# Performance work log

Hardware: AMD Instinct MI355X
Metric: run time of the kernel (lower is better)

Reference implementation:

```python
import jax, jax.numpy as jnp
import numpy as np

L, B, D = 2048, 8, 1024


def setup_inputs() -> dict:
    key = jax.random.key(0)
    ks = jax.random.split(key, 10)
    s = 0.02  # Linear weight scale to keep exp(k) in a sane range
    return {
        "x": jax.random.normal(ks[0], (L, B, D), jnp.float32),
        "mu_k": jax.random.uniform(ks[1], (D,), jnp.float32),
        "mu_v": jax.random.uniform(ks[2], (D,), jnp.float32),
        "mu_r": jax.random.uniform(ks[3], (D,), jnp.float32),
        "Wk": jax.random.normal(ks[4], (D, D), jnp.float32) * s,
        "Wv": jax.random.normal(ks[5], (D, D), jnp.float32) * s,
        "Wr": jax.random.normal(ks[6], (D, D), jnp.float32) * s,
        "W_out": jax.random.normal(ks[7], (D, D), jnp.float32) * s,
        "w": jax.random.uniform(ks[8], (D,), jnp.float32),
        "u": jax.random.uniform(ks[9], (D,), jnp.float32),
    }


def reference(x, mu_k, mu_v, mu_r, Wk, Wv, Wr, W_out, w, u):
    # x: [L, B, D] (time-first). Fresh hidden state => numerator/denominator_last = 0.
    Lx = x.shape[0]
    # PreviousMixing (RWKV token shift): mu*x_t + (1-mu)*x_{t-1}, zero initial prev.
    x_prev = jnp.concatenate([jnp.zeros_like(x[:1]), x[:-1]], axis=0)
    k = (mu_k * x + (1.0 - mu_k) * x_prev) @ Wk.T
    v = (mu_v * x + (1.0 - mu_v) * x_prev) @ Wv.T
    r = (mu_r * x + (1.0 - mu_r) * x_prev) @ Wr.T

    w_neg = -jnp.exp(w)                      # [D], negative decay
    exp_w = jnp.exp(w_neg)                   # [D]
    t = jnp.arange(Lx, dtype=x.dtype)
    ewp = jnp.exp(w_neg[None, :] * t[:, None])  # [L, D] decay progression

    exp_k = jnp.exp(k)                       # [L, B, D]
    exp_k_v = exp_k * v

    n = 2 * Lx  # zero-padded FFT length for linear convolution
    f_ewp = jnp.fft.rfft(ewp, n=n, axis=0)[:, None, :]        # [n/2+1, 1, D]
    f_ek = jnp.fft.rfft(exp_k, n=n, axis=0)                   # [n/2+1, B, D]
    f_ekv = jnp.fft.rfft(exp_k_v, n=n, axis=0)
    conv_ek = jnp.fft.irfft(f_ewp * f_ek, axis=0)[:Lx]         # [L, B, D]
    conv_ekv = jnp.fft.irfft(f_ewp * f_ekv, axis=0)[:Lx]

    # Initial numerator_last/denominator_last are zeros, so their terms vanish.
    denominator = conv_ek
    numerator = conv_ekv

    exp_u = jnp.exp(u)
    denominator_out = (denominator - exp_k) / exp_w + exp_k * exp_u
    numerator_out = (numerator - exp_k_v) / exp_w + exp_k_v * exp_u
    return (jax.nn.sigmoid(r) * numerator_out / denominator_out) @ W_out.T
```

## Files before the change

kernel.cpp:

```cpp
#include <hip/hip_runtime.h>
#include <cstddef>
#include <cstdint>

#define Lq 2048
#define Bq 8
#define Dq 1024
#define Mq (Lq*Bq)

typedef _Float16 f16;
typedef _Float16 f16x2 __attribute__((ext_vector_type(2)));
typedef _Float16 f16x8 __attribute__((ext_vector_type(8)));
typedef float f32x4 __attribute__((ext_vector_type(4)));

typedef const __attribute__((address_space(1))) uint32_t GU32;
typedef __attribute__((address_space(3))) uint32_t LU32;

#define BAR()    asm volatile("s_barrier" ::: "memory")
#define WAITV4() asm volatile("s_waitcnt vmcnt(4)" ::: "memory")

__global__ __launch_bounds__(256) void cvt3_k(const float* __restrict__ a,
                                              const float* __restrict__ b,
                                              const float* __restrict__ c,
                                              f16* __restrict__ dst) {
  int i = (blockIdx.x * 256 + threadIdx.x) * 8;
  const float* s = (blockIdx.y == 0) ? a : (blockIdx.y == 1) ? b : c;
  f16* d = dst + (size_t)blockIdx.y * ((size_t)Dq * Dq) + i;
  float4 v0 = *(const float4*)(s + i);
  float4 v1 = *(const float4*)(s + i + 4);
  f16x8 o;
  o[0] = (f16)v0.x; o[1] = (f16)v0.y; o[2] = (f16)v0.z; o[3] = (f16)v0.w;
  o[4] = (f16)v1.x; o[5] = (f16)v1.y; o[6] = (f16)v1.z; o[7] = (f16)v1.w;
  *(f16x8*)d = o;
}

__global__ __launch_bounds__(256) void cvt1_k(const float* __restrict__ s,
                                              f16* __restrict__ d) {
  int i = (blockIdx.x * 256 + threadIdx.x) * 8;
  float4 v0 = *(const float4*)(s + i);
  float4 v1 = *(const float4*)(s + i + 4);
  f16x8 o;
  o[0] = (f16)v0.x; o[1] = (f16)v0.y; o[2] = (f16)v0.z; o[3] = (f16)v0.w;
  o[4] = (f16)v1.x; o[5] = (f16)v1.y; o[6] = (f16)v1.z; o[7] = (f16)v1.w;
  *(f16x8*)(d + i) = o;
}

__global__ __launch_bounds__(256) void prep_k(const float* __restrict__ x,
                                              const float* __restrict__ muk,
                                              const float* __restrict__ muv,
                                              const float* __restrict__ mur,
                                              f16* __restrict__ xk,
                                              f16* __restrict__ xv,
                                              f16* __restrict__ xr) {
  const size_t base0 = ((size_t)blockIdx.x * 256 + threadIdx.x) * 8;
  const int col = (int)(base0 & (Dq - 1));

  float mk[8], mv[8], mr[8];
#define LD8(MU, DST)                                                           \
  { float4 m0 = *(const float4*)((MU) + col);                                  \
    float4 m1 = *(const float4*)((MU) + col + 4);                              \
    DST[0]=m0.x; DST[1]=m0.y; DST[2]=m0.z; DST[3]=m0.w;                        \
    DST[4]=m1.x; DST[5]=m1.y; DST[6]=m1.z; DST[7]=m1.w; }
  LD8(muk, mk) LD8(muv, mv) LD8(mur, mr)
#undef LD8

#pragma unroll
  for (int it = 0; it < 4; ++it) {
    size_t i = base0 + (size_t)it * (8u * 524288u);
    float4 a0 = *(const float4*)(x + i);
    float4 a1 = *(const float4*)(x + i + 4);
    float4 p0 = make_float4(0.f, 0.f, 0.f, 0.f), p1 = p0;
    if (i >= (size_t)(Bq * Dq)) {
      p0 = *(const float4*)(x + i - Bq * Dq);
      p1 = *(const float4*)(x + i - Bq * Dq + 4);
    }
    float av[8] = {a0.x, a0.y, a0.z, a0.w, a1.x, a1.y, a1.z, a1.w};
    float pv[8] = {p0.x, p0.y, p0.z, p0.w, p1.x, p1.y, p1.z, p1.w};
#define MIX8(MV, DST)                                                          \
    { f16x8 o;                                                                 \
      _Pragma("unroll")                                                        \
      for (int j = 0; j < 8; ++j) o[j] = (f16)(pv[j] + MV[j] * (av[j] - pv[j]));\
      *(f16x8*)((DST) + i) = o; }
    MIX8(mk, xk)
    MIX8(mv, xv)
    MIX8(mr, xr)
#undef MIX8
  }
}

template<int OUTF32>
__device__ __forceinline__ void gemm_core(const f16* __restrict__ A,
                                          const f16* __restrict__ W,
                                          void* __restrict__ Cv,
                                          int bx, int by) {
  __shared__ f16 lds[2][2][256][64];
  const int tid  = threadIdx.x;
  const int lane = tid & 63;
  const int wid  = tid >> 6;
  const int wr   = wid >> 2;
  const int wc   = wid & 3;

  const int fr = lane & 15;
  const int fg = lane >> 4;
  const int c0 = ((fg    ) ^ (fr & 7)) * 8;
  const int c1 = ((fg ^ 4) ^ (fr & 7)) * 8;

  const int rowoff = wid * 8 + (lane >> 3);
  const int scol   = ((lane & 7) ^ (lane >> 3)) * 8;
  const f16* Ab = A + (size_t)(by * 256) * Dq;
  const f16* Wb = W + (size_t)(bx * 256) * Dq;

#define STAGE(bufi, op, h, base, kt) do {                                      \
    const f16* _g = (base) + (size_t)((h) * 128 + rowoff) * Dq + (kt) * 64 + scol; \
    __builtin_amdgcn_global_load_lds((GU32*)_g,                                \
        (LU32*)&lds[bufi][op][(h) * 128 + wid * 8][0], 16, 0, 0);              \
    __builtin_amdgcn_global_load_lds((GU32*)(_g + (size_t)64 * Dq),            \
        (LU32*)&lds[bufi][op][(h) * 128 + 64 + wid * 8][0], 16, 0, 0);         \
  } while (0)

  f16x8 af[4][2], bf0[2][2], bf1[2][2];
  f32x4 acc[8][4] = {};

#define LOAD_A(bufi, mh)                                                       \
  _Pragma("unroll")                                                            \
  for (int mi2 = 0; mi2 < 4; ++mi2) {                                          \
    af[mi2][0] = *(const f16x8*)&lds[bufi][0][wr * 128 + (mh) * 64 + mi2 * 16 + fr][c0]; \
    af[mi2][1] = *(const f16x8*)&lds[bufi][0][wr * 128 + (mh) * 64 + mi2 * 16 + fr][c1]; \
  }
#define LOAD_B(bufi, nh, bf)                                                   \
  _Pragma("unroll")                                                            \
  for (int ni2 = 0; ni2 < 2; ++ni2) {                                          \
    bf[ni2][0] = *(const f16x8*)&lds[bufi][1][wc * 64 + (nh) * 32 + ni2 * 16 + fr][c0]; \
    bf[ni2][1] = *(const f16x8*)&lds[bufi][1][wc * 64 + (nh) * 32 + ni2 * 16 + fr][c1]; \
  }
#define MFMA_Q(mh, nh, bf)                                                     \
  __builtin_amdgcn_s_setprio(1);                                               \
  _Pragma("unroll")                                                            \
  for (int ks = 0; ks < 2; ++ks)                                               \
    _Pragma("unroll")                                                          \
    for (int mi2 = 0; mi2 < 4; ++mi2)                                          \
      _Pragma("unroll")                                                        \
      for (int ni2 = 0; ni2 < 2; ++ni2)                                        \
        acc[(mh) * 4 + mi2][(nh) * 2 + ni2] =                                  \
            __builtin_amdgcn_mfma_f32_16x16x32_f16(af[mi2][ks], bf[ni2][ks],   \
                acc[(mh) * 4 + mi2][(nh) * 2 + ni2], 0, 0, 0);                 \
  __builtin_amdgcn_s_setprio(0);

  STAGE(0, 0, 0, Ab, 0); STAGE(0, 0, 1, Ab, 0);
  STAGE(0, 1, 0, Wb, 0); STAGE(0, 1, 1, Wb, 0);
  STAGE(1, 1, 0, Wb, 1); STAGE(1, 1, 1, Wb, 1);
  WAITV4();
  BAR();

  for (int i = 0; i < 8; ++i) {
    const int t1 = 2 * i + 1;
    int t2 = 2 * i + 2; if (t2 > 15) t2 = 15;
    int t3 = 2 * i + 3; if (t3 > 15) t3 = 15;
    LOAD_A(0, 0); LOAD_B(0, 0, bf0);
    STAGE(1, 0, 0, Ab, t1);
    BAR(); MFMA_Q(0, 0, bf0); BAR();
    LOAD_B(0, 1, bf1);
    STAGE(1, 0, 1, Ab, t1);
    BAR(); MFMA_Q(0, 1, bf1); BAR();
    LOAD_A(0, 1);
    STAGE(0, 1, 0, Wb, t2);
    BAR(); MFMA_Q(1, 1, bf1); BAR();
    STAGE(0, 1, 1, Wb, t2);
    BAR(); MFMA_Q(1, 0, bf0); WAITV4(); BAR();
    LOAD_A(1, 0); LOAD_B(1, 0, bf0);
    STAGE(0, 0, 0, Ab, t2);
    BAR(); MFMA_Q(0, 0, bf0); BAR();
    LOAD_B(1, 1, bf1);
    STAGE(0, 0, 1, Ab, t2);
    BAR(); MFMA_Q(0, 1, bf1); BAR();
    LOAD_A(1, 1);
    STAGE(1, 1, 0, Wb, t3);
    BAR(); MFMA_Q(1, 1, bf1); BAR();
    STAGE(1, 1, 1, Wb, t3);
    BAR(); MFMA_Q(1, 0, bf0); WAITV4(); BAR();
  }

#pragma unroll
  for (int mi = 0; mi < 8; ++mi) {
    const int row0 = by * 256 + wr * 128 + mi * 16 + fg * 4;
#pragma unroll
    for (int ni = 0; ni < 4; ++ni) {
      const int col = bx * 256 + wc * 64 + ni * 16 + fr;
      if (OUTF32) {
        float* C = (float*)Cv;
#pragma unroll
        for (int j = 0; j < 4; ++j)
          C[(size_t)(row0 + j) * Dq + col] = acc[mi][ni][j];
      } else {
        f16* C = (f16*)Cv;
#pragma unroll
        for (int j = 0; j < 4; ++j)
          C[(size_t)(row0 + j) * Dq + col] = (f16)acc[mi][ni][j];
      }
    }
  }
#undef STAGE
#undef LOAD_A
#undef LOAD_B
#undef MFMA_Q
}

__global__ __launch_bounds__(512, 2) void gemm3_k(const f16* __restrict__ xr,
                                                  const f16* __restrict__ xv,
                                                  const f16* __restrict__ xk,
                                                  const f16* __restrict__ w16,
                                                  f16* __restrict__ rb,
                                                  f16* __restrict__ vb,
                                                  f16* __restrict__ kb) {
  const int s = blockIdx.x >> 8;
  const int inner = blockIdx.x & 255;
  const int wg = (inner & 7) * 32 + (inner >> 3);
  const f16* A = (s == 0) ? xr : (s == 1) ? xv : xk;
  const f16* W = w16 + (size_t)s * Dq * Dq;
  f16* C = (s == 0) ? rb : (s == 1) ? vb : kb;
  gemm_core<0>(A, W, C, wg & 3, wg >> 2);
}

__global__ __launch_bounds__(512, 2) void gemmO_k(const f16* __restrict__ A,
                                                  const f16* __restrict__ W,
                                                  float* __restrict__ C) {
  const int wg = (blockIdx.x & 7) * 32 + (blockIdx.x >> 3);
  gemm_core<1>(A, W, C, wg & 3, wg >> 2);
}

constexpr int CHUNK = 32, LOOKBACK = 16;

__global__ __launch_bounds__(256) void scan_k(const f16* __restrict__ kk,
                                              const f16* __restrict__ vv,
                                              const f16* rr,
                                              const float* __restrict__ w,
                                              const float* __restrict__ u,
                                              f16* y) {
  const int unit = blockIdx.y * 256 + threadIdx.x;
  const int d = (unit & 511) * 2;
  const int b = unit >> 9;
  const int t0 = blockIdx.x * CHUNK;

  const float dec0 = __expf(-__expf(w[d]));
  const float dec1 = __expf(-__expf(w[d + 1]));
  const float eu0  = __expf(u[d]);
  const float eu1  = __expf(u[d + 1]);

  float A0 = 0.f, A1 = 0.f, Av0 = 0.f, Av1 = 0.f;
  const size_t base = (size_t)b * Dq + d;

  if (t0 > 0) {
#pragma unroll
    for (int t = t0 - LOOKBACK; t < t0; ++t) {
      size_t idx = (size_t)t * (Bq * Dq) + base;
      f16x2 k2 = *(const f16x2*)(kk + idx);
      f16x2 v2 = *(const f16x2*)(vv + idx);
      float ek0 = __expf((float)k2[0]), ek1 = __expf((float)k2[1]);
      A0  = fmaf(dec0, A0,  ek0);
      A1  = fmaf(dec1, A1,  ek1);
      Av0 = fmaf(dec0, Av0, ek0 * (float)v2[0]);
      Av1 = fmaf(dec1, Av1, ek1 * (float)v2[1]);
    }
  }
#pragma unroll
  for (int t = t0; t < t0 + CHUNK; ++t) {
    size_t idx = (size_t)t * (Bq * Dq) + base;
    f16x2 k2 = *(const f16x2*)(kk + idx);
    f16x2 v2 = *(const f16x2*)(vv + idx);
    f16x2 r2 = *(const f16x2*)(rr + idx);
    float ek0 = __expf((float)k2[0]), ek1 = __expf((float)k2[1]);
    float ekv0 = ek0 * (float)v2[0], ekv1 = ek1 * (float)v2[1];
    float den0 = fmaf(ek0,  eu0, A0),  den1 = fmaf(ek1,  eu1, A1);
    float num0 = fmaf(ekv0, eu0, Av0), num1 = fmaf(ekv1, eu1, Av1);
    float s0 = __builtin_amdgcn_rcpf(1.f + __expf(-(float)r2[0]));
    float s1 = __builtin_amdgcn_rcpf(1.f + __expf(-(float)r2[1]));
    f16x2 o;
    o[0] = (f16)(s0 * num0 * __builtin_amdgcn_rcpf(den0));
    o[1] = (f16)(s1 * num1 * __builtin_amdgcn_rcpf(den1));
    *(f16x2*)(y + idx) = o;
    A0  = fmaf(dec0, A0,  ek0);
    A1  = fmaf(dec1, A1,  ek1);
    Av0 = fmaf(dec0, Av0, ekv0);
    Av1 = fmaf(dec1, Av1, ekv1);
  }
}

extern "C" void kernel_launch(void* const* d_in, const int* in_sizes, int n_in,
                              void* d_out, int out_size, void* d_ws, size_t ws_size,
                              hipStream_t stream) {
  const float* x    = (const float*)d_in[0];
  const float* mu_k = (const float*)d_in[1];
  const float* mu_v = (const float*)d_in[2];
  const float* mu_r = (const float*)d_in[3];
  const float* Wk   = (const float*)d_in[4];
  const float* Wv   = (const float*)d_in[5];
  const float* Wr   = (const float*)d_in[6];
  const float* Wo   = (const float*)d_in[7];
  const float* w    = (const float*)d_in[8];
  const float* u    = (const float*)d_in[9];

  f16* xk = (f16*)d_ws;
  f16* xv = xk + (size_t)Mq * Dq;
  f16* xr = xv + (size_t)Mq * Dq;
  f16* kb = xr + (size_t)Mq * Dq;
  f16* vb = kb + (size_t)Mq * Dq;
  f16* rb = vb + (size_t)Mq * Dq;
  f16* w16  = (f16*)d_out;
  f16* wo16 = xk;

  cvt3_k<<<dim3(512, 3), 256, 0, stream>>>(Wr, Wv, Wk, w16);
  prep_k<<<2048, 256, 0, stream>>>(x, mu_k, mu_v, mu_r, xk, xv, xr);
  gemm3_k<<<768, 512, 0, stream>>>(xr, xv, xk, w16, rb, vb, kb);
  cvt1_k<<<512, 256, 0, stream>>>(Wo, wo16);
  scan_k<<<dim3(Lq / CHUNK, 16), 256, 0, stream>>>(kb, vb, rb, w, u, rb);
  gemmO_k<<<256, 512, 0, stream>>>(rb, wo16, (float*)d_out);
}
```

Before: 218.2 us.

## Interleave r/v/k inputs and weights so one block computes all three projections

The three mixed activations and the three projection weights are now stored interleaved along a 3072-wide row, and the first GEMM launches 256 blocks instead of 768. Each block loops over the three projections, streams K-tiles continuously across projection boundaries and writes each output before resetting its accumulators. This cuts block launch and prologue overhead and keeps the pipeline running through the transitions. In exchange it gives a third as many blocks, one wave at 256 workgroups, so there is less parallel slack and the tail or load balance could get worse.

```diff
diff --git a/kernel.cpp b/kernel.cpp
--- a/kernel.cpp
+++ b/kernel.cpp
@@ -6,6 +6,7 @@
 #define Bq 8
 #define Dq 1024
 #define Mq (Lq*Bq)
+#define K3 3072
 
 typedef _Float16 f16;
 typedef _Float16 f16x2 __attribute__((ext_vector_type(2)));
@@ -21,10 +22,11 @@
 __global__ __launch_bounds__(256) void cvt3_k(const float* __restrict__ a,
                                               const float* __restrict__ b,
                                               const float* __restrict__ c,
-                                              f16* __restrict__ dst) {
+                                              f16* __restrict__ w3) {
   int i = (blockIdx.x * 256 + threadIdx.x) * 8;
   const float* s = (blockIdx.y == 0) ? a : (blockIdx.y == 1) ? b : c;
-  f16* d = dst + (size_t)blockIdx.y * ((size_t)Dq * Dq) + i;
+  int n = i >> 10, col = i & (Dq - 1);
+  f16* d = w3 + (size_t)n * K3 + blockIdx.y * Dq + col;
   float4 v0 = *(const float4*)(s + i);
   float4 v1 = *(const float4*)(s + i + 4);
   f16x8 o;
@@ -48,9 +50,7 @@
                                               const float* __restrict__ muk,
                                               const float* __restrict__ muv,
                                               const float* __restrict__ mur,
-                                              f16* __restrict__ xk,
-                                              f16* __restrict__ xv,
-                                              f16* __restrict__ xr) {
+                                              f16* __restrict__ x3) {
   const size_t base0 = ((size_t)blockIdx.x * 256 + threadIdx.x) * 8;
   const int col = (int)(base0 & (Dq - 1));
 
@@ -65,7 +65,9 @@
 
 #pragma unroll
   for (int it = 0; it < 4; ++it) {
-    size_t i = base0 + (size_t)it * (8u * 524288u);
+    size_t i = base0 + (size_t)it * 4194304u;
+    size_t m = i >> 10;
+    f16* dst = x3 + m * K3 + col;
     float4 a0 = *(const float4*)(x + i);
     float4 a1 = *(const float4*)(x + i + 4);
     float4 p0 = make_float4(0.f, 0.f, 0.f, 0.f), p1 = p0;
@@ -75,22 +77,22 @@
     }
     float av[8] = {a0.x, a0.y, a0.z, a0.w, a1.x, a1.y, a1.z, a1.w};
     float pv[8] = {p0.x, p0.y, p0.z, p0.w, p1.x, p1.y, p1.z, p1.w};
-#define MIX8(MV, DST)                                                          \
+#define MIX8(MV, OFF)                                                          \
     { f16x8 o;                                                                 \
       _Pragma("unroll")                                                        \
       for (int j = 0; j < 8; ++j) o[j] = (f16)(pv[j] + MV[j] * (av[j] - pv[j]));\
-      *(f16x8*)((DST) + i) = o; }
-    MIX8(mk, xk)
-    MIX8(mv, xv)
-    MIX8(mr, xr)
+      *(f16x8*)(dst + (OFF)) = o; }
+    MIX8(mr, 0)
+    MIX8(mv, Dq)
+    MIX8(mk, 2 * Dq)
 #undef MIX8
   }
 }
 
-template<int OUTF32>
+template<int OUTF32, int NEP, int AST>
 __device__ __forceinline__ void gemm_core(const f16* __restrict__ A,
                                           const f16* __restrict__ W,
-                                          void* __restrict__ Cv,
+                                          void* c0v, void* c1v, void* c2v,
                                           int bx, int by) {
   __shared__ f16 lds[2][2][256][64];
   const int tid  = threadIdx.x;
@@ -106,14 +108,15 @@
 
   const int rowoff = wid * 8 + (lane >> 3);
   const int scol   = ((lane & 7) ^ (lane >> 3)) * 8;
-  const f16* Ab = A + (size_t)(by * 256) * Dq;
-  const f16* Wb = W + (size_t)(bx * 256) * Dq;
+  const f16* Ab = A + (size_t)(by * 256) * AST;
+  const f16* Wb = W + (size_t)(bx * 256) * AST;
+  const int NT = NEP * 16;
 
 #define STAGE(bufi, op, h, base, kt) do {                                      \
-    const f16* _g = (base) + (size_t)((h) * 128 + rowoff) * Dq + (kt) * 64 + scol; \
+    const f16* _g = (base) + (size_t)((h) * 128 + rowoff) * AST + (kt) * 64 + scol; \
     __builtin_amdgcn_global_load_lds((GU32*)_g,                                \
         (LU32*)&lds[bufi][op][(h) * 128 + wid * 8][0], 16, 0, 0);              \
-    __builtin_amdgcn_global_load_lds((GU32*)(_g + (size_t)64 * Dq),            \
+    __builtin_amdgcn_global_load_lds((GU32*)(_g + (size_t)64 * AST),           \
         (LU32*)&lds[bufi][op][(h) * 128 + 64 + wid * 8][0], 16, 0, 0);         \
   } while (0)
 
@@ -151,50 +154,54 @@
   WAITV4();
   BAR();
 
-  for (int i = 0; i < 8; ++i) {
-    const int t1 = 2 * i + 1;
-    int t2 = 2 * i + 2; if (t2 > 15) t2 = 15;
-    int t3 = 2 * i + 3; if (t3 > 15) t3 = 15;
-    LOAD_A(0, 0); LOAD_B(0, 0, bf0);
-    STAGE(1, 0, 0, Ab, t1);
-    BAR(); MFMA_Q(0, 0, bf0); BAR();
-    LOAD_B(0, 1, bf1);
-    STAGE(1, 0, 1, Ab, t1);
-    BAR(); MFMA_Q(0, 1, bf1); BAR();
-    LOAD_A(0, 1);
-    STAGE(0, 1, 0, Wb, t2);
-    BAR(); MFMA_Q(1, 1, bf1); BAR();
-    STAGE(0, 1, 1, Wb, t2);
-    BAR(); MFMA_Q(1, 0, bf0); WAITV4(); BAR();
-    LOAD_A(1, 0); LOAD_B(1, 0, bf0);
-    STAGE(0, 0, 0, Ab, t2);
-    BAR(); MFMA_Q(0, 0, bf0); BAR();
-    LOAD_B(1, 1, bf1);
-    STAGE(0, 0, 1, Ab, t2);
-    BAR(); MFMA_Q(0, 1, bf1); BAR();
-    LOAD_A(1, 1);
-    STAGE(1, 1, 0, Wb, t3);
-    BAR(); MFMA_Q(1, 1, bf1); BAR();
-    STAGE(1, 1, 1, Wb, t3);
-    BAR(); MFMA_Q(1, 0, bf0); WAITV4(); BAR();
-  }
-
-#pragma unroll
-  for (int mi = 0; mi < 8; ++mi) {
-    const int row0 = by * 256 + wr * 128 + mi * 16 + fg * 4;
-#pragma unroll
-    for (int ni = 0; ni < 4; ++ni) {
-      const int col = bx * 256 + wc * 64 + ni * 16 + fr;
-      if (OUTF32) {
-        float* C = (float*)Cv;
-#pragma unroll
-        for (int j = 0; j < 4; ++j)
-          C[(size_t)(row0 + j) * Dq + col] = acc[mi][ni][j];
-      } else {
-        f16* C = (f16*)Cv;
-#pragma unroll
-        for (int j = 0; j < 4; ++j)
-          C[(size_t)(row0 + j) * Dq + col] = (f16)acc[mi][ni][j];
+  for (int e = 0; e < NEP; ++e) {
+    for (int i = 0; i < 8; ++i) {
+      const int g = e * 8 + i;
+      const int t1 = 2 * g + 1;
+      int t2 = 2 * g + 2; if (t2 > NT - 1) t2 = NT - 1;
+      int t3 = 2 * g + 3; if (t3 > NT - 1) t3 = NT - 1;
+      LOAD_A(0, 0); LOAD_B(0, 0, bf0);
+      STAGE(1, 0, 0, Ab, t1);
+      BAR(); MFMA_Q(0, 0, bf0); BAR();
+      LOAD_B(0, 1, bf1);
+      STAGE(1, 0, 1, Ab, t1);
+      BAR(); MFMA_Q(0, 1, bf1); BAR();
+      LOAD_A(0, 1);
+      STAGE(0, 1, 0, Wb, t2);
+      BAR(); MFMA_Q(1, 1, bf1); BAR();
+      STAGE(0, 1, 1, Wb, t2);
+      BAR(); MFMA_Q(1, 0, bf0); WAITV4(); BAR();
+      LOAD_A(1, 0); LOAD_B(1, 0, bf0);
+      STAGE(0, 0, 0, Ab, t2);
+      BAR(); MFMA_Q(0, 0, bf0); BAR();
+      LOAD_B(1, 1, bf1);
+      STAGE(0, 0, 1, Ab, t2);
+      BAR(); MFMA_Q(0, 1, bf1); BAR();
+      LOAD_A(1, 1);
+      STAGE(1, 1, 0, Wb, t3);
+      BAR(); MFMA_Q(1, 1, bf1); BAR();
+      STAGE(1, 1, 1, Wb, t3);
+      BAR(); MFMA_Q(1, 0, bf0); WAITV4(); BAR();
+    }
+    void* Cv = (e == 0) ? c0v : (e == 1) ? c1v : c2v;
+#pragma unroll
+    for (int mi = 0; mi < 8; ++mi) {
+      const int row0 = by * 256 + wr * 128 + mi * 16 + fg * 4;
+#pragma unroll
+      for (int ni = 0; ni < 4; ++ni) {
+        const int col = bx * 256 + wc * 64 + ni * 16 + fr;
+        if (OUTF32) {
+          float* C = (float*)Cv;
+#pragma unroll
+          for (int j = 0; j < 4; ++j)
+            C[(size_t)(row0 + j) * Dq + col] = acc[mi][ni][j];
+        } else {
+          f16* C = (f16*)Cv;
+#pragma unroll
+          for (int j = 0; j < 4; ++j)
+            C[(size_t)(row0 + j) * Dq + col] = (f16)acc[mi][ni][j];
+        }
+        acc[mi][ni] = (f32x4){0.f, 0.f, 0.f, 0.f};
       }
     }
   }
@@ -204,27 +211,20 @@
 #undef MFMA_Q
 }
 
-__global__ __launch_bounds__(512, 2) void gemm3_k(const f16* __restrict__ xr,
-                                                  const f16* __restrict__ xv,
-                                                  const f16* __restrict__ xk,
-                                                  const f16* __restrict__ w16,
+__global__ __launch_bounds__(512, 2) void gemm3_k(const f16* __restrict__ x3,
+                                                  const f16* __restrict__ w3,
                                                   f16* __restrict__ rb,
                                                   f16* __restrict__ vb,
                                                   f16* __restrict__ kb) {
-  const int s = blockIdx.x >> 8;
-  const int inner = blockIdx.x & 255;
-  const int wg = (inner & 7) * 32 + (inner >> 3);
-  const f16* A = (s == 0) ? xr : (s == 1) ? xv : xk;
-  const f16* W = w16 + (size_t)s * Dq * Dq;
-  f16* C = (s == 0) ? rb : (s == 1) ? vb : kb;
-  gemm_core<0>(A, W, C, wg & 3, wg >> 2);
+  const int wg = (blockIdx.x & 7) * 32 + (blockIdx.x >> 3);
+  gemm_core<0, 3, K3>(x3, w3, rb, vb, kb, wg & 3, wg >> 2);
 }
 
 __global__ __launch_bounds__(512, 2) void gemmO_k(const f16* __restrict__ A,
                                                   const f16* __restrict__ W,
                                                   float* __restrict__ C) {
   const int wg = (blockIdx.x & 7) * 32 + (blockIdx.x >> 3);
-  gemm_core<1>(A, W, C, wg & 3, wg >> 2);
+  gemm_core<1, 1, Dq>(A, W, C, nullptr, nullptr, wg & 3, wg >> 2);
 }
 
 constexpr int CHUNK = 32, LOOKBACK = 16;
@@ -298,18 +298,16 @@
   const float* w    = (const float*)d_in[8];
   const float* u    = (const float*)d_in[9];
 
-  f16* xk = (f16*)d_ws;
-  f16* xv = xk + (size_t)Mq * Dq;
-  f16* xr = xv + (size_t)Mq * Dq;
-  f16* kb = xr + (size_t)Mq * Dq;
+  f16* x3 = (f16*)d_ws;
+  f16* kb = x3 + (size_t)Mq * K3;
   f16* vb = kb + (size_t)Mq * Dq;
   f16* rb = vb + (size_t)Mq * Dq;
-  f16* w16  = (f16*)d_out;
-  f16* wo16 = xk;
-
-  cvt3_k<<<dim3(512, 3), 256, 0, stream>>>(Wr, Wv, Wk, w16);
-  prep_k<<<2048, 256, 0, stream>>>(x, mu_k, mu_v, mu_r, xk, xv, xr);
-  gemm3_k<<<768, 512, 0, stream>>>(xr, xv, xk, w16, rb, vb, kb);
+  f16* w3   = (f16*)d_out;
+  f16* wo16 = x3;
+
+  cvt3_k<<<dim3(512, 3), 256, 0, stream>>>(Wr, Wv, Wk, w3);
+  prep_k<<<2048, 256, 0, stream>>>(x, mu_k, mu_v, mu_r, x3);
+  gemm3_k<<<256, 512, 0, stream>>>(x3, w3, rb, vb, kb);
   cvt1_k<<<512, 256, 0, stream>>>(Wo, wo16);
   scan_k<<<dim3(Lq / CHUNK, 16), 256, 0, stream>>>(kb, vb, rb, w, u, rb);
   gemmO_k<<<256, 512, 0, stream>>>(rb, wo16, (float*)d_out);
```

Result: slower. 234.3 us (+7.4%).

## Restructure GEMM mainloop to 4-slot K=32 LDS pipeline with prefetch depth three

Applied to the files above, without the earlier changes.

The f16 GEMM core now uses four LDS ring slots of 256x32 tiles for A and B instead of two 256x64 buffers. Loads run three K-steps ahead and the wait count is raised to vmcnt(8). Fragment loads and MFMA phases are reorganised to one k-slice per phase with a new XOR swizzle. The aim is to hide global-load latency better with deeper prefetch, at the cost of more barriers per unit of K work and smaller MFMA bursts between syncs.

```diff
diff --git a/kernel.cpp b/kernel.cpp
--- a/kernel.cpp
+++ b/kernel.cpp
@@ -16,7 +16,7 @@
 typedef __attribute__((address_space(3))) uint32_t LU32;
 
 #define BAR()    asm volatile("s_barrier" ::: "memory")
-#define WAITV4() asm volatile("s_waitcnt vmcnt(4)" ::: "memory")
+#define WAITV8() asm volatile("s_waitcnt vmcnt(8)" ::: "memory")
 
 __global__ __launch_bounds__(256) void cvt3_k(const float* __restrict__ a,
                                               const float* __restrict__ b,
@@ -65,7 +65,7 @@
 
 #pragma unroll
   for (int it = 0; it < 4; ++it) {
-    size_t i = base0 + (size_t)it * (8u * 524288u);
+    size_t i = base0 + (size_t)it * 4194304u;
     float4 a0 = *(const float4*)(x + i);
     float4 a1 = *(const float4*)(x + i + 4);
     float4 p0 = make_float4(0.f, 0.f, 0.f, 0.f), p1 = p0;
@@ -92,7 +92,8 @@
                                           const f16* __restrict__ W,
                                           void* __restrict__ Cv,
                                           int bx, int by) {
-  __shared__ f16 lds[2][2][256][64];
+  __shared__ f16 As[4][256][32];
+  __shared__ f16 Bs[4][256][32];
   const int tid  = threadIdx.x;
   const int lane = tid & 63;
   const int wid  = tid >> 6;
@@ -101,82 +102,67 @@
 
   const int fr = lane & 15;
   const int fg = lane >> 4;
-  const int c0 = ((fg    ) ^ (fr & 7)) * 8;
-  const int c1 = ((fg ^ 4) ^ (fr & 7)) * 8;
-
-  const int rowoff = wid * 8 + (lane >> 3);
-  const int scol   = ((lane & 7) ^ (lane >> 3)) * 8;
-  const f16* Ab = A + (size_t)(by * 256) * Dq;
-  const f16* Wb = W + (size_t)(bx * 256) * Dq;
-
-#define STAGE(bufi, op, h, base, kt) do {                                      \
-    const f16* _g = (base) + (size_t)((h) * 128 + rowoff) * Dq + (kt) * 64 + scol; \
-    __builtin_amdgcn_global_load_lds((GU32*)_g,                                \
-        (LU32*)&lds[bufi][op][(h) * 128 + wid * 8][0], 16, 0, 0);              \
-    __builtin_amdgcn_global_load_lds((GU32*)(_g + (size_t)64 * Dq),            \
-        (LU32*)&lds[bufi][op][(h) * 128 + 64 + wid * 8][0], 16, 0, 0);         \
+  const int cA = (fg ^ ((fr >> 1) & 3)) * 8;
+
+  const int s_r = wid * 16 + (lane >> 2);
+  const int s_c = ((lane & 3) ^ ((lane >> 3) & 3)) * 8;
+  const f16* Ag = A + ((size_t)(by * 256 + s_r)) * Dq + s_c;
+  const f16* Wg = W + ((size_t)(bx * 256 + s_r)) * Dq + s_c;
+
+#define STAGE_A(slot, kt) do {                                                 \
+    __builtin_amdgcn_global_load_lds((GU32*)(Ag + (kt) * 32),                  \
+        (LU32*)&As[slot][wid * 16][0], 16, 0, 0);                              \
+    __builtin_amdgcn_global_load_lds((GU32*)(Ag + (size_t)128 * Dq + (kt) * 32),\
+        (LU32*)&As[slot][128 + wid * 16][0], 16, 0, 0);                        \
   } while (0)
-
-  f16x8 af[4][2], bf0[2][2], bf1[2][2];
+#define STAGE_B(slot, kt) do {                                                 \
+    __builtin_amdgcn_global_load_lds((GU32*)(Wg + (kt) * 32),                  \
+        (LU32*)&Bs[slot][wid * 16][0], 16, 0, 0);                              \
+    __builtin_amdgcn_global_load_lds((GU32*)(Wg + (size_t)128 * Dq + (kt) * 32),\
+        (LU32*)&Bs[slot][128 + wid * 16][0], 16, 0, 0);                        \
+  } while (0)
+
+  f16x8 af[4], bf[4];
   f32x4 acc[8][4] = {};
 
-#define LOAD_A(bufi, mh)                                                       \
+#define LOAD_A4(slot, mh)                                                      \
   _Pragma("unroll")                                                            \
-  for (int mi2 = 0; mi2 < 4; ++mi2) {                                          \
-    af[mi2][0] = *(const f16x8*)&lds[bufi][0][wr * 128 + (mh) * 64 + mi2 * 16 + fr][c0]; \
-    af[mi2][1] = *(const f16x8*)&lds[bufi][0][wr * 128 + (mh) * 64 + mi2 * 16 + fr][c1]; \
-  }
-#define LOAD_B(bufi, nh, bf)                                                   \
+  for (int mi2 = 0; mi2 < 4; ++mi2)                                            \
+    af[mi2] = *(const f16x8*)&As[slot][wr * 128 + (mh) * 64 + mi2 * 16 + fr][cA];
+#define LOAD_B4(slot)                                                          \
   _Pragma("unroll")                                                            \
-  for (int ni2 = 0; ni2 < 2; ++ni2) {                                          \
-    bf[ni2][0] = *(const f16x8*)&lds[bufi][1][wc * 64 + (nh) * 32 + ni2 * 16 + fr][c0]; \
-    bf[ni2][1] = *(const f16x8*)&lds[bufi][1][wc * 64 + (nh) * 32 + ni2 * 16 + fr][c1]; \
-  }
-#define MFMA_Q(mh, nh, bf)                                                     \
+  for (int ni2 = 0; ni2 < 4; ++ni2)                                            \
+    bf[ni2] = *(const f16x8*)&Bs[slot][wc * 64 + ni2 * 16 + fr][cA];
+#define MFMA_PH(mh)                                                            \
   __builtin_amdgcn_s_setprio(1);                                               \
   _Pragma("unroll")                                                            \
-  for (int ks = 0; ks < 2; ++ks)                                               \
+  for (int mi2 = 0; mi2 < 4; ++mi2)                                            \
     _Pragma("unroll")                                                          \
-    for (int mi2 = 0; mi2 < 4; ++mi2)                                          \
-      _Pragma("unroll")                                                        \
-      for (int ni2 = 0; ni2 < 2; ++ni2)                                        \
-        acc[(mh) * 4 + mi2][(nh) * 2 + ni2] =                                  \
-            __builtin_amdgcn_mfma_f32_16x16x32_f16(af[mi2][ks], bf[ni2][ks],   \
-                acc[(mh) * 4 + mi2][(nh) * 2 + ni2], 0, 0, 0);                 \
+    for (int ni2 = 0; ni2 < 4; ++ni2)                                          \
+      acc[(mh) * 4 + mi2][ni2] =                                               \
+          __builtin_amdgcn_mfma_f32_16x16x32_f16(af[mi2], bf[ni2],             \
+              acc[(mh) * 4 + mi2][ni2], 0, 0, 0);                              \
   __builtin_amdgcn_s_setprio(0);
 
-  STAGE(0, 0, 0, Ab, 0); STAGE(0, 0, 1, Ab, 0);
-  STAGE(0, 1, 0, Wb, 0); STAGE(0, 1, 1, Wb, 0);
-  STAGE(1, 1, 0, Wb, 1); STAGE(1, 1, 1, Wb, 1);
-  WAITV4();
+  STAGE_A(0, 0); STAGE_B(0, 0);
+  STAGE_A(1, 1); STAGE_B(1, 1);
+  STAGE_A(2, 2); STAGE_B(2, 2);
+  WAITV8();
   BAR();
 
-  for (int i = 0; i < 8; ++i) {
-    const int t1 = 2 * i + 1;
-    int t2 = 2 * i + 2; if (t2 > 15) t2 = 15;
-    int t3 = 2 * i + 3; if (t3 > 15) t3 = 15;
-    LOAD_A(0, 0); LOAD_B(0, 0, bf0);
-    STAGE(1, 0, 0, Ab, t1);
-    BAR(); MFMA_Q(0, 0, bf0); BAR();
-    LOAD_B(0, 1, bf1);
-    STAGE(1, 0, 1, Ab, t1);
-    BAR(); MFMA_Q(0, 1, bf1); BAR();
-    LOAD_A(0, 1);
-    STAGE(0, 1, 0, Wb, t2);
-    BAR(); MFMA_Q(1, 1, bf1); BAR();
-    STAGE(0, 1, 1, Wb, t2);
-    BAR(); MFMA_Q(1, 0, bf0); WAITV4(); BAR();
-    LOAD_A(1, 0); LOAD_B(1, 0, bf0);
-    STAGE(0, 0, 0, Ab, t2);
-    BAR(); MFMA_Q(0, 0, bf0); BAR();
-    LOAD_B(1, 1, bf1);
-    STAGE(0, 0, 1, Ab, t2);
-    BAR(); MFMA_Q(0, 1, bf1); BAR();
-    LOAD_A(1, 1);
-    STAGE(1, 1, 0, Wb, t3);
-    BAR(); MFMA_Q(1, 1, bf1); BAR();
-    STAGE(1, 1, 1, Wb, t3);
-    BAR(); MFMA_Q(1, 0, bf0); WAITV4(); BAR();
+  for (int tt = 0; tt < 8; ++tt) {
+#pragma unroll
+    for (int q = 0; q < 4; ++q) {
+      const int t = tt * 4 + q;
+      int st = t + 3; if (st > 31) st = 31;
+      const int ss = (q + 3) & 3;
+      LOAD_A4(q, 0); LOAD_B4(q);
+      STAGE_A(ss, st);
+      BAR(); MFMA_PH(0); BAR();
+      LOAD_A4(q, 1);
+      STAGE_B(ss, st);
+      BAR(); MFMA_PH(1); WAITV8(); BAR();
+    }
   }
 
 #pragma unroll
@@ -198,10 +184,11 @@
       }
     }
   }
-#undef STAGE
-#undef LOAD_A
-#undef LOAD_B
-#undef MFMA_Q
+#undef STAGE_A
+#undef STAGE_B
+#undef LOAD_A4
+#undef LOAD_B4
+#undef MFMA_PH
 }
 
 __global__ __launch_bounds__(512, 2) void gemm3_k(const f16* __restrict__ xr,
```

Result: slower. 228.2 us (+4.6%).

## Fold weight conversion into prep kernel and retile output GEMM to 128x256

Applied to the files above, without the earlier changes.

The separate fp32-to-fp16 conversion of Wr/Wv/Wk is merged into the token-shift prep kernel as extra blocks, removing one launch. The output projection GEMM gets its own kernel with 128x256 tiles, K-step 32, double-buffered global-to-LDS loads and a smaller LDS footprint. It launches 512 workgroups instead of 256, which is meant to fill the CUs better. Smaller tiles give less data reuse per workgroup in exchange.

```diff
diff --git a/kernel.cpp b/kernel.cpp
--- a/kernel.cpp
+++ b/kernel.cpp
@@ -17,41 +17,34 @@
 
 #define BAR()    asm volatile("s_barrier" ::: "memory")
 #define WAITV4() asm volatile("s_waitcnt vmcnt(4)" ::: "memory")
-
-__global__ __launch_bounds__(256) void cvt3_k(const float* __restrict__ a,
-                                              const float* __restrict__ b,
-                                              const float* __restrict__ c,
-                                              f16* __restrict__ dst) {
-  int i = (blockIdx.x * 256 + threadIdx.x) * 8;
-  const float* s = (blockIdx.y == 0) ? a : (blockIdx.y == 1) ? b : c;
-  f16* d = dst + (size_t)blockIdx.y * ((size_t)Dq * Dq) + i;
-  float4 v0 = *(const float4*)(s + i);
-  float4 v1 = *(const float4*)(s + i + 4);
-  f16x8 o;
-  o[0] = (f16)v0.x; o[1] = (f16)v0.y; o[2] = (f16)v0.z; o[3] = (f16)v0.w;
-  o[4] = (f16)v1.x; o[5] = (f16)v1.y; o[6] = (f16)v1.z; o[7] = (f16)v1.w;
-  *(f16x8*)d = o;
-}
-
-__global__ __launch_bounds__(256) void cvt1_k(const float* __restrict__ s,
-                                              f16* __restrict__ d) {
-  int i = (blockIdx.x * 256 + threadIdx.x) * 8;
-  float4 v0 = *(const float4*)(s + i);
-  float4 v1 = *(const float4*)(s + i + 4);
-  f16x8 o;
-  o[0] = (f16)v0.x; o[1] = (f16)v0.y; o[2] = (f16)v0.z; o[3] = (f16)v0.w;
-  o[4] = (f16)v1.x; o[5] = (f16)v1.y; o[6] = (f16)v1.z; o[7] = (f16)v1.w;
-  *(f16x8*)(d + i) = o;
-}
+#define WAITV3() asm volatile("s_waitcnt vmcnt(3)" ::: "memory")
 
 __global__ __launch_bounds__(256) void prep_k(const float* __restrict__ x,
                                               const float* __restrict__ muk,
                                               const float* __restrict__ muv,
                                               const float* __restrict__ mur,
+                                              const float* __restrict__ Wr,
+                                              const float* __restrict__ Wv,
+                                              const float* __restrict__ Wk,
                                               f16* __restrict__ xk,
                                               f16* __restrict__ xv,
-                                              f16* __restrict__ xr) {
-  const size_t base0 = ((size_t)blockIdx.x * 256 + threadIdx.x) * 8;
+                                              f16* __restrict__ xr,
+                                              f16* __restrict__ w16) {
+  const int bid = blockIdx.x;
+  if (bid < 1536) {
+    int y = bid >> 9;
+    int i = ((bid & 511) * 256 + threadIdx.x) * 8;
+    const float* s = (y == 0) ? Wr : (y == 1) ? Wv : Wk;
+    f16* d = w16 + (size_t)y * ((size_t)Dq * Dq) + i;
+    float4 v0 = *(const float4*)(s + i);
+    float4 v1 = *(const float4*)(s + i + 4);
+    f16x8 o;
+    o[0] = (f16)v0.x; o[1] = (f16)v0.y; o[2] = (f16)v0.z; o[3] = (f16)v0.w;
+    o[4] = (f16)v1.x; o[5] = (f16)v1.y; o[6] = (f16)v1.z; o[7] = (f16)v1.w;
+    *(f16x8*)d = o;
+    return;
+  }
+  const size_t base0 = ((size_t)(bid - 1536) * 256 + threadIdx.x) * 8;
   const int col = (int)(base0 & (Dq - 1));
 
   float mk[8], mv[8], mr[8];
@@ -65,7 +58,7 @@
 
 #pragma unroll
   for (int it = 0; it < 4; ++it) {
-    size_t i = base0 + (size_t)it * (8u * 524288u);
+    size_t i = base0 + (size_t)it * 4194304u;
     float4 a0 = *(const float4*)(x + i);
     float4 a1 = *(const float4*)(x + i + 4);
     float4 p0 = make_float4(0.f, 0.f, 0.f, 0.f), p1 = p0;
@@ -87,11 +80,21 @@
   }
 }
 
-template<int OUTF32>
-__device__ __forceinline__ void gemm_core(const f16* __restrict__ A,
-                                          const f16* __restrict__ W,
-                                          void* __restrict__ Cv,
-                                          int bx, int by) {
+__global__ __launch_bounds__(256) void cvt1_k(const float* __restrict__ s,
+                                              f16* __restrict__ d) {
+  int i = (blockIdx.x * 256 + threadIdx.x) * 8;
+  float4 v0 = *(const float4*)(s + i);
+  float4 v1 = *(const float4*)(s + i + 4);
+  f16x8 o;
+  o[0] = (f16)v0.x; o[1] = (f16)v0.y; o[2] = (f16)v0.z; o[3] = (f16)v0.w;
+  o[4] = (f16)v1.x; o[5] = (f16)v1.y; o[6] = (f16)v1.z; o[7] = (f16)v1.w;
+  *(f16x8*)(d + i) = o;
+}
+
+__device__ __forceinline__ void gemm_core8(const f16* __restrict__ A,
+                                           const f16* __restrict__ W,
+                                           f16* __restrict__ Cv,
+                                           int bx, int by) {
   __shared__ f16 lds[2][2][256][64];
   const int tid  = threadIdx.x;
   const int lane = tid & 63;
@@ -185,17 +188,9 @@
 #pragma unroll
     for (int ni = 0; ni < 4; ++ni) {
       const int col = bx * 256 + wc * 64 + ni * 16 + fr;
-      if (OUTF32) {
-        float* C = (float*)Cv;
-#pragma unroll
-        for (int j = 0; j < 4; ++j)
-          C[(size_t)(row0 + j) * Dq + col] = acc[mi][ni][j];
-      } else {
-        f16* C = (f16*)Cv;
-#pragma unroll
-        for (int j = 0; j < 4; ++j)
-          C[(size_t)(row0 + j) * Dq + col] = (f16)acc[mi][ni][j];
-      }
+#pragma unroll
+      for (int j = 0; j < 4; ++j)
+        Cv[(size_t)(row0 + j) * Dq + col] = (f16)acc[mi][ni][j];
     }
   }
 #undef STAGE
@@ -217,14 +212,85 @@
   const f16* A = (s == 0) ? xr : (s == 1) ? xv : xk;
   const f16* W = w16 + (size_t)s * Dq * Dq;
   f16* C = (s == 0) ? rb : (s == 1) ? vb : kb;
-  gemm_core<0>(A, W, C, wg & 3, wg >> 2);
-}
-
-__global__ __launch_bounds__(512, 2) void gemmO_k(const f16* __restrict__ A,
+  gemm_core8(A, W, C, wg & 3, wg >> 2);
+}
+
+__global__ __launch_bounds__(512, 4) void gemmO_k(const f16* __restrict__ A,
                                                   const f16* __restrict__ W,
                                                   float* __restrict__ C) {
-  const int wg = (blockIdx.x & 7) * 32 + (blockIdx.x >> 3);
-  gemm_core<1>(A, W, C, wg & 3, wg >> 2);
+  const int wg = (blockIdx.x & 7) * 64 + (blockIdx.x >> 3);
+  const int bx = wg & 3, by = wg >> 2;
+
+  __shared__ f16 As[2][128][32];
+  __shared__ f16 Bs[2][256][32];
+  const int tid  = threadIdx.x;
+  const int lane = tid & 63;
+  const int wid  = tid >> 6;
+  const int wr   = wid >> 2;
+  const int wc   = wid & 3;
+
+  const int fr = lane & 15;
+  const int fg = lane >> 4;
+  const int cA = (fg ^ ((fr >> 1) & 3)) * 8;
+
+  const int s_r = wid * 16 + (lane >> 2);
+  const int s_c = ((lane & 3) ^ ((lane >> 3) & 3)) * 8;
+  const f16* Ag = A + ((size_t)(by * 128 + s_r)) * Dq + s_c;
+  const f16* Wg = W + ((size_t)(bx * 256 + s_r)) * Dq + s_c;
+
+#define STAGEO(slot, kt) do {                                                  \
+    __builtin_amdgcn_global_load_lds((GU32*)(Ag + (kt) * 32),                  \
+        (LU32*)&As[slot][wid * 16][0], 16, 0, 0);                              \
+    __builtin_amdgcn_global_load_lds((GU32*)(Wg + (kt) * 32),                  \
+        (LU32*)&Bs[slot][wid * 16][0], 16, 0, 0);                              \
+    __builtin_amdgcn_global_load_lds((GU32*)(Wg + (size_t)128 * Dq + (kt) * 32),\
+        (LU32*)&Bs[slot][128 + wid * 16][0], 16, 0, 0);                        \
+  } while (0)
+
+  f16x8 af[4], bf[4];
+  f32x4 acc[4][4] = {};
+
+#define TILEO(q, t) do {                                                       \
+    int st = (t) + 1; if (st > 31) st = 31;                                    \
+    STAGEO((q) ^ 1, st);                                                       \
+    WAITV3();                                                                  \
+    BAR();                                                                     \
+    _Pragma("unroll")                                                          \
+    for (int mi = 0; mi < 4; ++mi)                                             \
+      af[mi] = *(const f16x8*)&As[q][wr * 64 + mi * 16 + fr][cA];              \
+    _Pragma("unroll")                                                          \
+    for (int ni = 0; ni < 4; ++ni)                                             \
+      bf[ni] = *(const f16x8*)&Bs[q][wc * 64 + ni * 16 + fr][cA];              \
+    __builtin_amdgcn_s_setprio(1);                                             \
+    _Pragma("unroll")                                                          \
+    for (int mi = 0; mi < 4; ++mi)                                             \
+      _Pragma("unroll")                                                        \
+      for (int ni = 0; ni < 4; ++ni)                                           \
+        acc[mi][ni] = __builtin_amdgcn_mfma_f32_16x16x32_f16(af[mi], bf[ni],   \
+                          acc[mi][ni], 0, 0, 0);                               \
+    __builtin_amdgcn_s_setprio(0);                                             \
+    BAR();                                                                     \
+  } while (0)
+
+  STAGEO(0, 0);
+  for (int tt = 0; tt < 16; ++tt) {
+    TILEO(0, 2 * tt);
+    TILEO(1, 2 * tt + 1);
+  }
+
+#pragma unroll
+  for (int mi = 0; mi < 4; ++mi) {
+    const int row0 = by * 128 + wr * 64 + mi * 16 + fg * 4;
+#pragma unroll
+    for (int ni = 0; ni < 4; ++ni) {
+      const int col = bx * 256 + wc * 64 + ni * 16 + fr;
+#pragma unroll
+      for (int j = 0; j < 4; ++j)
+        C[(size_t)(row0 + j) * Dq + col] = acc[mi][ni][j];
+    }
+  }
+#undef STAGEO
+#undef TILEO
 }
 
 constexpr int CHUNK = 32, LOOKBACK = 16;
@@ -307,10 +373,10 @@
   f16* w16  = (f16*)d_out;
   f16* wo16 = xk;
 
-  cvt3_k<<<dim3(512, 3), 256, 0, stream>>>(Wr, Wv, Wk, w16);
-  prep_k<<<2048, 256, 0, stream>>>(x, mu_k, mu_v, mu_r, xk, xv, xr);
+  prep_k<<<3584, 256, 0, stream>>>(x, mu_k, mu_v, mu_r, Wr, Wv, Wk,
+                                   xk, xv, xr, w16);
   gemm3_k<<<768, 512, 0, stream>>>(xr, xv, xk, w16, rb, vb, kb);
   cvt1_k<<<512, 256, 0, stream>>>(Wo, wo16);
   scan_k<<<dim3(Lq / CHUNK, 16), 256, 0, stream>>>(kb, vb, rb, w, u, rb);
-  gemmO_k<<<256, 512, 0, stream>>>(rb, wo16, (float*)d_out);
-}
+  gemmO_k<<<512, 512, 0, stream>>>(rb, wo16, (float*)d_out);
+}
```

Measured after the change: 220.2 us. Within noise of the previous version (+0.9%).
